# Kernel tuning notes

Hardware: AMD Instinct MI355X
Metric: run time of the kernel (lower is better)

The kernel has to match this reference:

```python
import math
import jax, jax.numpy as jnp
import numpy as np

L = 16
T = 2 ** 19
F = 2
N_MIN = 16
N_MAX = 512
BOUND = 3.0
BATCH = 524288

_b = math.exp((math.log(N_MAX) - math.log(N_MIN)) / (L - 1))
NS = np.array([int(N_MIN * _b ** i) for i in range(L)], dtype=np.float32)  # resolutions per level
PRIMES = np.array([1, 2654435761, 805459861], dtype=np.uint32)
# 8 cube-corner offsets (x,y,z) in {0,1}
OFFSETS = np.array([[x, y, z] for x in (0, 1) for y in (0, 1) for z in (0, 1)], dtype=np.uint32)


def setup_inputs() -> dict:
    key = jax.random.key(0)
    k_pos, k_tab = jax.random.split(key)
    inputs = jax.random.uniform(k_pos, (BATCH, 3), dtype=jnp.float32, minval=-BOUND, maxval=BOUND)
    hash_table = jax.random.uniform(k_tab, (L, T, F), dtype=jnp.float32) * 0.0002 - 0.0001
    return {"inputs": inputs, "hash_table": hash_table}


def reference(inputs, hash_table):
    x = (inputs + BOUND) / (2 * BOUND)                      # [B,3] in [0,1]
    widths = jnp.asarray(1.0 / NS)[:, None, None]           # [L,1,1], width = 1/n per level
    pmin = jnp.floor(x[None] / widths)                      # [L,B,3] floor cell coord (== torch //)
    per = (x[None] - pmin * widths) / widths                # [L,B,3] fractional position in cell
    offs = jnp.asarray(OFFSETS)                             # [8,3] uint32
    corners = pmin.astype(jnp.uint32)[:, :, None, :] + offs[None, None]  # [L,B,8,3]
    prod = corners * jnp.asarray(PRIMES)                    # uint32 mul wraps mod 2^32
    idx = (prod[..., 0] ^ prod[..., 1] ^ prod[..., 2]) % jnp.uint32(T)   # [L,B,8]
    feats = jax.vmap(lambda tab, i: tab[i])(hash_table, idx)             # [L,B,8,F] gathers
    # trilinear weights: use per where offset bit is 1, (1-per) where 0
    w = jnp.prod(jnp.where(offs[None, None].astype(bool), per[:, :, None, :], 1.0 - per[:, :, None, :]), axis=-1)  # [L,B,8]
    feat = jnp.einsum('lbcf,lbc->lbf', feats, w)            # [L,B,F]
    B = inputs.shape[0]
    return feat.transpose(1, 0, 2).reshape(B, L * F)
```

## Files before the change

kernel.cpp:

```cpp
#include <hip/hip_runtime.h>
#include <cstdint>
#include <cstddef>


#define NUM_LEVELS 16
#define TBL_MASK ((1u << 19) - 1u)
#define PRIME_Y 2654435761u
#define PRIME_Z 805459861u
#define BATCH 524288

typedef float nfloat4 __attribute__((ext_vector_type(4)));

__constant__ float c_ns[NUM_LEVELS] = {
    16.f, 20.f, 25.f, 32.f, 40.f, 50.f, 64.f, 80.f,
    101.f, 128.f, 161.f, 203.f, 256.f, 322.f, 406.f, 512.f
};

struct Corner8 {
    uint32_t i[8];
    float wx0, wy0, wz0;
};

__device__ __forceinline__ float2 d2f2(double d) {
    union { double d; float2 f; } u;
    u.d = d;
    return u.f;
}

__device__ __forceinline__ double f22d(float2 f) {
    union { double d; float2 f; } u;
    u.f = f;
    return u.d;
}

__device__ __forceinline__ Corner8 corner_setup_xyz(
    float xs, float ys, float zs, float n)
{
    const float tx = xs * n, ty = ys * n, tz = zs * n;
    const float fpx = floorf(tx), fpy = floorf(ty), fpz = floorf(tz);

    Corner8 c;
    c.wx0 = tx - fpx;
    c.wy0 = ty - fpy;
    c.wz0 = tz - fpz;

    const uint32_t px = (uint32_t)fpx;
    const uint32_t py = (uint32_t)fpy;
    const uint32_t pz = (uint32_t)fpz;

    const uint32_t hx0 = px;
    const uint32_t hx1 = px + 1u;
    const uint32_t hy0 = py * PRIME_Y;
    const uint32_t hy1 = hy0 + PRIME_Y;
    const uint32_t hz0 = pz * PRIME_Z;
    const uint32_t hz1 = hz0 + PRIME_Z;

    c.i[0] = (hx0 ^ hy0 ^ hz0) & TBL_MASK;
    c.i[1] = (hx0 ^ hy0 ^ hz1) & TBL_MASK;
    c.i[2] = (hx0 ^ hy1 ^ hz0) & TBL_MASK;
    c.i[3] = (hx0 ^ hy1 ^ hz1) & TBL_MASK;
    c.i[4] = (hx1 ^ hy0 ^ hz0) & TBL_MASK;
    c.i[5] = (hx1 ^ hy0 ^ hz1) & TBL_MASK;
    c.i[6] = (hx1 ^ hy1 ^ hz0) & TBL_MASK;
    c.i[7] = (hx1 ^ hy1 ^ hz1) & TBL_MASK;
    return c;
}

__device__ __forceinline__ float2 blend(const Corner8& c, const float2 f[8])
{
    const float wx1 = c.wx0, wx0 = 1.0f - c.wx0;
    const float wy1 = c.wy0, wy0 = 1.0f - c.wy0;
    const float wz1 = c.wz0, wz0 = 1.0f - c.wz0;

    float a0 = 0.0f, a1 = 0.0f, w;
    w = wx0 * wy0 * wz0; a0 = fmaf(f[0].x, w, a0); a1 = fmaf(f[0].y, w, a1);
    w = wx0 * wy0 * wz1; a0 = fmaf(f[1].x, w, a0); a1 = fmaf(f[1].y, w, a1);
    w = wx0 * wy1 * wz0; a0 = fmaf(f[2].x, w, a0); a1 = fmaf(f[2].y, w, a1);
    w = wx0 * wy1 * wz1; a0 = fmaf(f[3].x, w, a0); a1 = fmaf(f[3].y, w, a1);
    w = wx1 * wy0 * wz0; a0 = fmaf(f[4].x, w, a0); a1 = fmaf(f[4].y, w, a1);
    w = wx1 * wy0 * wz1; a0 = fmaf(f[5].x, w, a0); a1 = fmaf(f[5].y, w, a1);
    w = wx1 * wy1 * wz0; a0 = fmaf(f[6].x, w, a0); a1 = fmaf(f[6].y, w, a1);
    w = wx1 * wy1 * wz1; a0 = fmaf(f[7].x, w, a0); a1 = fmaf(f[7].y, w, a1);
    return make_float2(a0, a1);
}

__global__ __launch_bounds__(256) void enc_level_kernel(
    const float* __restrict__ in,
    const float* __restrict__ table,
    double* __restrict__ ws,
    int base_level)
{
    const int slot = blockIdx.x & 7;
    const int chunk = blockIdx.x >> 3;
    const int l = base_level + slot;
    const int p = chunk * 256 + threadIdx.x;

    const float vx = __builtin_nontemporal_load(&in[p * 3 + 0]);
    const float vy = __builtin_nontemporal_load(&in[p * 3 + 1]);
    const float vz = __builtin_nontemporal_load(&in[p * 3 + 2]);
    const float xs = (vx + 3.0f) / 6.0f;
    const float ys = (vy + 3.0f) / 6.0f;
    const float zs = (vz + 3.0f) / 6.0f;

    const Corner8 c = corner_setup_xyz(xs, ys, zs, c_ns[l]);

    const double* __restrict__ tb = ((const double*)table) + ((size_t)l << 19);

    float2 f[8];
#pragma unroll
    for (int k = 0; k < 8; ++k) f[k] = d2f2(tb[c.i[k]]);

    __builtin_nontemporal_store(f22d(blend(c, f)), &ws[(size_t)l * BATCH + p]);
}

__global__ __launch_bounds__(256) void transpose_kernel(
    const double* __restrict__ ws,
    nfloat4* __restrict__ out)
{
    __shared__ double lds[256][NUM_LEVELS + 1];

    const int tid = threadIdx.x;
    const int p0 = blockIdx.x * 256;

#pragma unroll
    for (int l = 0; l < NUM_LEVELS; ++l) {
        lds[tid][l] = __builtin_nontemporal_load(&ws[(size_t)l * BATCH + p0 + tid]);
    }
    __syncthreads();

#pragma unroll
    for (int it = 0; it < 8; ++it) {
        const int e = it * 256 + tid;
        const int p = e >> 3;
        const int j = e & 7;
        const float2 a = d2f2(lds[p][2 * j]);
        const float2 b = d2f2(lds[p][2 * j + 1]);
        nfloat4 r;
        r.x = a.x; r.y = a.y; r.z = b.x; r.w = b.y;
        __builtin_nontemporal_store(r, &out[(size_t)blockIdx.x * 2048 + e]);
    }
}

__global__ __launch_bounds__(256) void enc_scatter_kernel(
    const float* __restrict__ in,
    const float* __restrict__ table,
    float2* __restrict__ out)
{
    const int v = blockIdx.x & 15;
    const int chunk = blockIdx.x >> 4;
    const int l = (v < 8) ? (15 - v) : (v - 8);
    const int p = chunk * 256 + threadIdx.x;

    const float vx = in[p * 3 + 0];
    const float vy = in[p * 3 + 1];
    const float vz = in[p * 3 + 2];
    const Corner8 c = corner_setup_xyz((vx + 3.0f) / 6.0f, (vy + 3.0f) / 6.0f,
                                       (vz + 3.0f) / 6.0f, c_ns[l]);
    const double* __restrict__ tb = ((const double*)table) + ((size_t)l << 19);
    float2 f[8];
#pragma unroll
    for (int k = 0; k < 8; ++k) f[k] = d2f2(tb[c.i[k]]);
    out[(size_t)p * NUM_LEVELS + l] = blend(c, f);
}

extern "C" void kernel_launch(void* const* d_in, const int* in_sizes, int n_in,
                              void* d_out, int out_size, void* d_ws, size_t ws_size,
                              hipStream_t stream) {
    const float* inputs = (const float*)d_in[0];
    const float* table  = (const float*)d_in[1];

    const size_t ws_needed = (size_t)NUM_LEVELS * BATCH * sizeof(float2);

    if (ws_size >= ws_needed) {
        double* ws = (double*)d_ws;
        enc_level_kernel<<<16384, 256, 0, stream>>>(inputs, table, ws, 8);
        enc_level_kernel<<<16384, 256, 0, stream>>>(inputs, table, ws, 0);
        transpose_kernel<<<2048, 256, 0, stream>>>(ws, (nfloat4*)d_out);
    } else {
        enc_scatter_kernel<<<32768, 256, 0, stream>>>(inputs, table, (float2*)d_out);
    }
}
```

Measured before the change: 411.8 us.

## Replace per-level launches with persistent atomic work-stealing kernel and paired corner loads

Replaces the two per-level encoding launches with one persistent kernel of 2048 blocks. Each wave grabs 64-point work units from atomic counters. Each slot's block group is pinned to a share of the fine levels (6-15), and the coarse levels (0-5) are drained from shared pools afterwards. The intent is to balance load across levels and keep each level's hash table localised to a subset of CUs/XCDs. Corner lookups now use 16-byte paired loads that fetch the x+1 neighbour too when px is even, which cuts the number of gather loads. The counters are placed in the output buffer, which the transpose later overwrites. This adds an init launch and atomic traffic.

```diff
diff --git a/kernel.cpp b/kernel.cpp
--- a/kernel.cpp
+++ b/kernel.cpp
@@ -8,30 +8,208 @@
 #define PRIME_Y 2654435761u
 #define PRIME_Z 805459861u
 #define BATCH 524288
+#define PINNED_TOTAL 10240
+#define COARSE_POOL 6144
 
 typedef float nfloat4 __attribute__((ext_vector_type(4)));
+typedef double ndouble2 __attribute__((ext_vector_type(2)));
 
 __constant__ float c_ns[NUM_LEVELS] = {
     16.f, 20.f, 25.f, 32.f, 40.f, 50.f, 64.f, 80.f,
     101.f, 128.f, 161.f, 203.f, 256.f, 322.f, 406.f, 512.f
 };
 
+typedef struct { int level; int base; int count; } Seg;
+__constant__ Seg c_pinned[8][2] = {
+    {{ 6,    0, 8192}, { 7,    0, 2048}},
+    {{ 7, 2048, 6144}, { 8,    0, 4096}},
+    {{ 8, 4096, 4096}, { 9,    0, 6144}},
+    {{ 9, 6144, 2048}, {10,    0, 8192}},
+    {{11,    0, 8192}, {12,    0, 2048}},
+    {{12, 2048, 6144}, {13,    0, 4096}},
+    {{13, 4096, 4096}, {14,    0, 6144}},
+    {{14, 6144, 2048}, {15,    0, 8192}},
+};
+
+__device__ __forceinline__ float2 d2f2(double d) {
+    union { double d; float2 f; } u;
+    u.d = d;
+    return u.f;
+}
+
+__device__ __forceinline__ double f22d(float2 f) {
+    union { double d; float2 f; } u;
+    u.f = f;
+    return u.d;
+}
+
+__device__ __forceinline__ void process_unit(
+    int l, int unit, int lane,
+    const float* __restrict__ in,
+    const float* __restrict__ table,
+    double* __restrict__ ws)
+{
+    const int p = unit * 64 + lane;
+    const float vx = __builtin_nontemporal_load(&in[p * 3 + 0]);
+    const float vy = __builtin_nontemporal_load(&in[p * 3 + 1]);
+    const float vz = __builtin_nontemporal_load(&in[p * 3 + 2]);
+    const float xs = (vx + 3.0f) / 6.0f;
+    const float ys = (vy + 3.0f) / 6.0f;
+    const float zs = (vz + 3.0f) / 6.0f;
+    const float n = c_ns[l];
+    const float tx = xs * n, ty = ys * n, tz = zs * n;
+    const float fpx = floorf(tx), fpy = floorf(ty), fpz = floorf(tz);
+    const float wx1 = tx - fpx, wy1 = ty - fpy, wz1 = tz - fpz;
+    const uint32_t px = (uint32_t)fpx;
+    const uint32_t py = (uint32_t)fpy;
+    const uint32_t pz = (uint32_t)fpz;
+
+    const uint32_t hy0 = py * PRIME_Y, hy1 = hy0 + PRIME_Y;
+    const uint32_t hz0 = pz * PRIME_Z, hz1 = hz0 + PRIME_Z;
+    const uint32_t b0 = hy0 ^ hz0, b1 = hy0 ^ hz1;
+    const uint32_t b2 = hy1 ^ hz0, b3 = hy1 ^ hz1;
+
+    const uint32_t i00 = (px ^ b0) & TBL_MASK;
+    const uint32_t i01 = (px ^ b1) & TBL_MASK;
+    const uint32_t i02 = (px ^ b2) & TBL_MASK;
+    const uint32_t i03 = (px ^ b3) & TBL_MASK;
+    const uint32_t qx = px + 1u;
+    const uint32_t i40 = (qx ^ b0) & TBL_MASK;
+    const uint32_t i41 = (qx ^ b1) & TBL_MASK;
+    const uint32_t i42 = (qx ^ b2) & TBL_MASK;
+    const uint32_t i43 = (qx ^ b3) & TBL_MASK;
+
+    const double* __restrict__ tb = ((const double*)table) + ((size_t)l << 19);
+    const ndouble2* __restrict__ tb2 = (const ndouble2*)tb;
+
+    const ndouble2 q0 = tb2[i00 >> 1];
+    const ndouble2 q1 = tb2[i01 >> 1];
+    const ndouble2 q2 = tb2[i02 >> 1];
+    const ndouble2 q3 = tb2[i03 >> 1];
+
+    const bool odd = (px & 1u) != 0u;
+    double g0 = 0.0, g1 = 0.0, g2 = 0.0, g3 = 0.0;
+    if (odd) {
+        g0 = tb[i40];
+        g1 = tb[i41];
+        g2 = tb[i42];
+        g3 = tb[i43];
+    }
+
+    const double e00 = (i00 & 1u) ? q0.y : q0.x;
+    const double e01 = (i01 & 1u) ? q1.y : q1.x;
+    const double e02 = (i02 & 1u) ? q2.y : q2.x;
+    const double e03 = (i03 & 1u) ? q3.y : q3.x;
+    const double p00 = (i00 & 1u) ? q0.x : q0.y;
+    const double p01 = (i01 & 1u) ? q1.x : q1.y;
+    const double p02 = (i02 & 1u) ? q2.x : q2.y;
+    const double p03 = (i03 & 1u) ? q3.x : q3.y;
+
+    float2 f[8];
+    f[0] = d2f2(e00); f[1] = d2f2(e01); f[2] = d2f2(e02); f[3] = d2f2(e03);
+    f[4] = d2f2(odd ? g0 : p00);
+    f[5] = d2f2(odd ? g1 : p01);
+    f[6] = d2f2(odd ? g2 : p02);
+    f[7] = d2f2(odd ? g3 : p03);
+
+    const float wx0 = 1.0f - wx1;
+    const float wy0 = 1.0f - wy1;
+    const float wz0 = 1.0f - wz1;
+
+    float a0 = 0.0f, a1 = 0.0f, w;
+    w = wx0 * wy0 * wz0; a0 = fmaf(f[0].x, w, a0); a1 = fmaf(f[0].y, w, a1);
+    w = wx0 * wy0 * wz1; a0 = fmaf(f[1].x, w, a0); a1 = fmaf(f[1].y, w, a1);
+    w = wx0 * wy1 * wz0; a0 = fmaf(f[2].x, w, a0); a1 = fmaf(f[2].y, w, a1);
+    w = wx0 * wy1 * wz1; a0 = fmaf(f[3].x, w, a0); a1 = fmaf(f[3].y, w, a1);
+    w = wx1 * wy0 * wz0; a0 = fmaf(f[4].x, w, a0); a1 = fmaf(f[4].y, w, a1);
+    w = wx1 * wy0 * wz1; a0 = fmaf(f[5].x, w, a0); a1 = fmaf(f[5].y, w, a1);
+    w = wx1 * wy1 * wz0; a0 = fmaf(f[6].x, w, a0); a1 = fmaf(f[6].y, w, a1);
+    w = wx1 * wy1 * wz1; a0 = fmaf(f[7].x, w, a0); a1 = fmaf(f[7].y, w, a1);
+
+    __builtin_nontemporal_store(f22d(make_float2(a0, a1)),
+                                &ws[(size_t)l * BATCH + p]);
+}
+
+__device__ __forceinline__ uint32_t wave_grab(uint32_t* ctr, int lane) {
+    uint32_t c = 0;
+    if (lane == 0) c = atomicAdd(ctr, 1u);
+    return (uint32_t)__shfl((int)c, 0);
+}
+
+__global__ __launch_bounds__(256) void enc_dyn_kernel(
+    const float* __restrict__ in,
+    const float* __restrict__ table,
+    double* __restrict__ ws,
+    uint32_t* __restrict__ ctr)
+{
+    const int slot = blockIdx.x & 7;
+    const int lane = threadIdx.x & 63;
+
+    {
+        uint32_t* pc = ctr + slot * 32;
+        const Seg s0 = c_pinned[slot][0];
+        const Seg s1 = c_pinned[slot][1];
+        uint32_t c = wave_grab(pc, lane);
+        while (c < PINNED_TOTAL) {
+            const uint32_t cn = wave_grab(pc, lane);
+            int level, unit;
+            if ((int)c < s0.count) { level = s0.level; unit = s0.base + (int)c; }
+            else                   { level = s1.level; unit = s1.base + (int)c - s0.count; }
+            process_unit(level, unit, lane, in, table, ws);
+            c = cn;
+        }
+    }
+
+    for (int k = 0; k < 8; ++k) {
+        const int pool = (slot + k) & 7;
+        uint32_t* pc = ctr + (8 + pool) * 32;
+        uint32_t c = wave_grab(pc, lane);
+        while (c < COARSE_POOL) {
+            const uint32_t cn = wave_grab(pc, lane);
+            const int level = 5 - (int)(c >> 10);
+            const int unit = (int)(c & 1023) + (pool << 10);
+            process_unit(level, unit, lane, in, table, ws);
+            c = cn;
+        }
+    }
+}
+
+__global__ __launch_bounds__(64) void init_ctr_kernel(uint32_t* ctr) {
+    if (threadIdx.x < 16) ctr[threadIdx.x * 32] = 0u;
+}
+
+__global__ __launch_bounds__(256) void transpose_kernel(
+    const double* __restrict__ ws,
+    nfloat4* __restrict__ out)
+{
+    __shared__ double lds[256][NUM_LEVELS + 1];
+
+    const int tid = threadIdx.x;
+    const int p0 = blockIdx.x * 256;
+
+#pragma unroll
+    for (int l = 0; l < NUM_LEVELS; ++l) {
+        lds[tid][l] = __builtin_nontemporal_load(&ws[(size_t)l * BATCH + p0 + tid]);
+    }
+    __syncthreads();
+
+#pragma unroll
+    for (int it = 0; it < 8; ++it) {
+        const int e = it * 256 + tid;
+        const int p = e >> 3;
+        const int j = e & 7;
+        const float2 a = d2f2(lds[p][2 * j]);
+        const float2 b = d2f2(lds[p][2 * j + 1]);
+        nfloat4 r;
+        r.x = a.x; r.y = a.y; r.z = b.x; r.w = b.y;
+        __builtin_nontemporal_store(r, &out[(size_t)blockIdx.x * 2048 + e]);
+    }
+}
+
 struct Corner8 {
     uint32_t i[8];
     float wx0, wy0, wz0;
 };
-
-__device__ __forceinline__ float2 d2f2(double d) {
-    union { double d; float2 f; } u;
-    u.d = d;
-    return u.f;
-}
-
-__device__ __forceinline__ double f22d(float2 f) {
-    union { double d; float2 f; } u;
-    u.f = f;
-    return u.d;
-}
 
 __device__ __forceinline__ Corner8 corner_setup_xyz(
     float xs, float ys, float zs, float n)
@@ -66,7 +244,7 @@
     return c;
 }
 
-__device__ __forceinline__ float2 blend(const Corner8& c, const float2 f[8])
+__device__ __forceinline__ float2 blend8(const Corner8& c, const float2 f[8])
 {
     const float wx1 = c.wx0, wx0 = 1.0f - c.wx0;
     const float wy1 = c.wy0, wy0 = 1.0f - c.wy0;
@@ -84,63 +262,6 @@
     return make_float2(a0, a1);
 }
 
-__global__ __launch_bounds__(256) void enc_level_kernel(
-    const float* __restrict__ in,
-    const float* __restrict__ table,
-    double* __restrict__ ws,
-    int base_level)
-{
-    const int slot = blockIdx.x & 7;
-    const int chunk = blockIdx.x >> 3;
-    const int l = base_level + slot;
-    const int p = chunk * 256 + threadIdx.x;
-
-    const float vx = __builtin_nontemporal_load(&in[p * 3 + 0]);
-    const float vy = __builtin_nontemporal_load(&in[p * 3 + 1]);
-    const float vz = __builtin_nontemporal_load(&in[p * 3 + 2]);
-    const float xs = (vx + 3.0f) / 6.0f;
-    const float ys = (vy + 3.0f) / 6.0f;
-    const float zs = (vz + 3.0f) / 6.0f;
-
-    const Corner8 c = corner_setup_xyz(xs, ys, zs, c_ns[l]);
-
-    const double* __restrict__ tb = ((const double*)table) + ((size_t)l << 19);
-
-    float2 f[8];
-#pragma unroll
-    for (int k = 0; k < 8; ++k) f[k] = d2f2(tb[c.i[k]]);
-
-    __builtin_nontemporal_store(f22d(blend(c, f)), &ws[(size_t)l * BATCH + p]);
-}
-
-__global__ __launch_bounds__(256) void transpose_kernel(
-    const double* __restrict__ ws,
-    nfloat4* __restrict__ out)
-{
-    __shared__ double lds[256][NUM_LEVELS + 1];
-
-    const int tid = threadIdx.x;
-    const int p0 = blockIdx.x * 256;
-
-#pragma unroll
-    for (int l = 0; l < NUM_LEVELS; ++l) {
-        lds[tid][l] = __builtin_nontemporal_load(&ws[(size_t)l * BATCH + p0 + tid]);
-    }
-    __syncthreads();
-
-#pragma unroll
-    for (int it = 0; it < 8; ++it) {
-        const int e = it * 256 + tid;
-        const int p = e >> 3;
-        const int j = e & 7;
-        const float2 a = d2f2(lds[p][2 * j]);
-        const float2 b = d2f2(lds[p][2 * j + 1]);
-        nfloat4 r;
-        r.x = a.x; r.y = a.y; r.z = b.x; r.w = b.y;
-        __builtin_nontemporal_store(r, &out[(size_t)blockIdx.x * 2048 + e]);
-    }
-}
-
 __global__ __launch_bounds__(256) void enc_scatter_kernel(
     const float* __restrict__ in,
     const float* __restrict__ table,
@@ -160,7 +281,7 @@
     float2 f[8];
 #pragma unroll
     for (int k = 0; k < 8; ++k) f[k] = d2f2(tb[c.i[k]]);
-    out[(size_t)p * NUM_LEVELS + l] = blend(c, f);
+    out[(size_t)p * NUM_LEVELS + l] = blend8(c, f);
 }
 
 extern "C" void kernel_launch(void* const* d_in, const int* in_sizes, int n_in,
@@ -173,8 +294,9 @@
 
     if (ws_size >= ws_needed) {
         double* ws = (double*)d_ws;
-        enc_level_kernel<<<16384, 256, 0, stream>>>(inputs, table, ws, 8);
-        enc_level_kernel<<<16384, 256, 0, stream>>>(inputs, table, ws, 0);
+        uint32_t* ctr = (uint32_t*)d_out;
+        init_ctr_kernel<<<1, 64, 0, stream>>>(ctr);
+        enc_dyn_kernel<<<2048, 256, 0, stream>>>(inputs, table, ws, ctr);
         transpose_kernel<<<2048, 256, 0, stream>>>(ws, (nfloat4*)d_out);
     } else {
         enc_scatter_kernel<<<32768, 256, 0, stream>>>(inputs, table, (float2*)d_out);
```

Result: slower. 544.0 us (+32.1%).
